# Kernel optimization log

Hardware: AMD Instinct MI355X
Metric: run time of the kernel (lower is better)

The kernel has to match this reference:

```python
import jax, jax.numpy as jnp
import numpy as np

NUM_HEADS = 12

def setup_inputs() -> dict:
    key = jax.random.key(0)
    k1, k2, k3, k4 = jax.random.split(key, 4)
    B, N, D = 8, 1024, 768
    x = jax.random.normal(k1, (B, N, D), dtype=jnp.float32)
    mask = jax.random.randint(k2, (B, N), 0, 2, dtype=jnp.int32)
    Wqkv = jax.random.normal(k3, (3 * D, D), dtype=jnp.float32) * (D ** -0.5)
    Wproj = jax.random.normal(k4, (D, D), dtype=jnp.float32) * (D ** -0.5)
    bproj = jnp.zeros((D,), dtype=jnp.float32)
    return {"x": x, "mask": mask, "Wqkv": Wqkv, "Wproj": Wproj, "bproj": bproj}

def reference(x, mask, Wqkv, Wproj, bproj):
    B, N, D = x.shape
    H = NUM_HEADS
    hd = D // H
    scale = hd ** -0.5
    # QKV projection (no bias), split into q,k,v of shape [B,H,N,hd]
    qkv = jnp.einsum('bnd,ed->bne', x, Wqkv).reshape(B, N, 3, H, hd)
    qkv = jnp.transpose(qkv, (2, 0, 3, 1, 4))
    q, k, v = qkv[0], qkv[1], qkv[2]
    # padding mask: attend where both query and key are valid; masked-out
    # (padded) query rows attend only to themselves (diagonal) to avoid NaNs
    m = mask.astype(bool)  # [B,N]
    pair = m[:, None, :, None] & m[:, None, None, :]          # [B,1,N,N]
    diag = jnp.eye(N, dtype=bool)[None, None]                 # [1,1,N,N]
    attn_mask = pair | (diag & ~m[:, None, :, None])          # [B,1,N,N]
    scores = jnp.einsum('bhnd,bhmd->bhnm', q, k) * scale      # [B,H,N,N]
    scores = jnp.where(attn_mask, scores, jnp.finfo(scores.dtype).min)
    attn = jax.nn.softmax(scores, axis=-1)
    out = jnp.einsum('bhnm,bhmd->bhnd', attn, v)
    out = jnp.transpose(out, (0, 2, 1, 3)).reshape(B, N, D)
    out = jnp.einsum('bnd,ed->bne', out, Wproj) + bproj
    return out
```

## Files before the change

### kernel.cpp

```cpp
#include <hip/hip_runtime.h>
#include <hip/hip_bf16.h>
#include <stdint.h>


typedef unsigned short u16;
typedef __attribute__((ext_vector_type(8))) short short8;
typedef __attribute__((ext_vector_type(4))) float f32x4;

#define MFMA16(a, b, c) __builtin_amdgcn_mfma_f32_16x16x32_bf16((a), (b), (c), 0, 0, 0)

static __device__ __forceinline__ float bf2f(u16 u) {
    return __uint_as_float(((unsigned int)u) << 16);
}
static __device__ __forceinline__ u16 f2bf(float f) {
    __hip_bfloat16 h = __float2bfloat16(f);
    return *(u16*)&h;
}
static __device__ __forceinline__ void gld16(const u16* g, u16* l) {
  __builtin_amdgcn_global_load_lds(
      (const __attribute__((address_space(1))) void*)g,
      (__attribute__((address_space(3))) void*)l, 16, 0, 0);
}

__global__ __launch_bounds__(256) void cvt_bf16(
    const float* __restrict__ s0, u16* __restrict__ d0, int n0,
    const float* __restrict__ s1, u16* __restrict__ d1, int n1,
    const float* __restrict__ s2, u16* __restrict__ d2, int n2) {
  int i = (blockIdx.x * 256 + threadIdx.x) * 4;
  const float* s; u16* d;
  if (i < n0) { s = s0 + i; d = d0 + i; }
  else if ((i -= n0) < n1) { s = s1 + i; d = d1 + i; }
  else if ((i -= n1) < n2) { s = s2 + i; d = d2 + i; }
  else return;
  float4 v = *(const float4*)s;
  ushort4 o;
  o.x = f2bf(v.x); o.y = f2bf(v.y); o.z = f2bf(v.z); o.w = f2bf(v.w);
  *(ushort4*)d = o;
}

template<int K, int LDC, bool BF16OUT>
__global__ __launch_bounds__(256) void gemm_bt(
    const u16* __restrict__ A,
    const u16* __restrict__ B,
    void* __restrict__ Cout,
    const float* __restrict__ bias) {
  __shared__ u16 As[128 * 32];
  __shared__ u16 Bs[128 * 32];
  const int tid = threadIdx.x;
  const int w = tid >> 6, l = tid & 63;
  const int lane16 = l & 15, quad = l >> 4;
  const int i0 = blockIdx.y * 128, j0 = blockIdx.x * 128;
  const int mh = (w & 1) * 64;
  const int nh = (w >> 1) * 64;

  f32x4 acc[4][4];
  #pragma unroll
  for (int mt = 0; mt < 4; mt++)
    #pragma unroll
    for (int nt = 0; nt < 4; nt++) acc[mt][nt] = (f32x4){0.f, 0.f, 0.f, 0.f};

  for (int kt = 0; kt < K / 32; kt++) {
    const int k0 = kt * 32;
    __syncthreads();
    #pragma unroll
    for (int s = 0; s < 2; s++) {
      int idx = tid + s * 256;
      int row = idx >> 2, c8 = (idx & 3) * 8;
      gld16(&A[(size_t)(i0 + row) * K + k0 + c8], &As[row * 32 + c8]);
      gld16(&B[(size_t)(j0 + row) * K + k0 + c8], &Bs[row * 32 + c8]);
    }
    __syncthreads();

    short8 af[4], bf[4];
    #pragma unroll
    for (int mt = 0; mt < 4; mt++)
      af[mt] = *(const short8*)&As[(mh + mt * 16 + lane16) * 32 + quad * 8];
    #pragma unroll
    for (int nt = 0; nt < 4; nt++)
      bf[nt] = *(const short8*)&Bs[(nh + nt * 16 + lane16) * 32 + quad * 8];
    #pragma unroll
    for (int mt = 0; mt < 4; mt++)
      #pragma unroll
      for (int nt = 0; nt < 4; nt++)
        acc[mt][nt] = MFMA16(af[mt], bf[nt], acc[mt][nt]);
  }

  #pragma unroll
  for (int mt = 0; mt < 4; mt++) {
    #pragma unroll
    for (int nt = 0; nt < 4; nt++) {
      int col = j0 + nh + nt * 16 + lane16;
      #pragma unroll
      for (int r = 0; r < 4; r++) {
        int row = i0 + mh + mt * 16 + quad * 4 + r;
        if (BF16OUT) {
          ((u16*)Cout)[(size_t)row * LDC + col] = f2bf(acc[mt][nt][r]);
        } else {
          ((float*)Cout)[(size_t)row * LDC + col] = acc[mt][nt][r] + bias[col];
        }
      }
    }
  }
}

__global__ __launch_bounds__(256, 4) void attn_mfma(
    const u16* __restrict__ qkv,
    const int* __restrict__ mask,
    u16* __restrict__ ctx) {
  __shared__ u16 Ks[64][72];
  __shared__ u16 Vt[64][72];
  __shared__ u16 Ps[4][32][72];
  __shared__ float mkb[64];
  __shared__ int mqs[128];

  const int tid = threadIdx.x;
  const int w = tid >> 6, l = tid & 63;
  const int lane16 = l & 15, quad = l >> 4;
  const int idx = blockIdx.x;
  const int bh = idx % 96;
  const int rb = idx / 96;
  const int b = bh / 12, h = bh % 12;
  const int n0 = rb * 128;
  const int baseRow = b * 1024;

  const int key_s = tid >> 2, ds_s = (tid & 3) * 16;
  const int kA_s = (tid & 31) * 2, dg_s = tid >> 5;

  if (tid < 128) mqs[tid] = mask[baseRow + n0 + tid];

  short8 qfrag[2][2];
  #pragma unroll
  for (int qt = 0; qt < 2; qt++) {
    const u16* qp = qkv + (size_t)(baseRow + n0 + w*32 + qt*16 + lane16) * 2304 + h*64;
    #pragma unroll
    for (int ks = 0; ks < 2; ks++)
      qfrag[qt][ks] = *(const short8*)(qp + ks*32 + quad*8);
  }

  f32x4 oacc[2][4];
  #pragma unroll
  for (int qt = 0; qt < 2; qt++)
    #pragma unroll
    for (int nt = 0; nt < 4; nt++) oacc[qt][nt] = (f32x4){0.f, 0.f, 0.f, 0.f};
  float lsum[2] = {0.f, 0.f};

  const float K1 = 0.18033688011112043f;
  const float K0 = -23.083120654223415f;

  for (int c = 0; c < 16; c++) {
    if (c) __syncthreads();
    {
      const u16* kp = qkv + (size_t)(baseRow + c*64 + key_s) * 2304 + 768 + h*64 + ds_s;
      uint4 kr0 = *(const uint4*)kp;
      uint4 kr1 = *(const uint4*)(kp + 8);
      const u16* vp = qkv + (size_t)(baseRow + c*64 + kA_s) * 2304 + 1536 + h*64 + dg_s*8;
      uint4 vr0 = *(const uint4*)vp;
      uint4 vr1 = *(const uint4*)(vp + 2304);
      *(uint4*)&Ks[key_s][ds_s]     = kr0;
      *(uint4*)&Ks[key_s][ds_s + 8] = kr1;
      const u16* va = (const u16*)&vr0;
      const u16* vb = (const u16*)&vr1;
      #pragma unroll
      for (int j = 0; j < 8; j++)
        *(unsigned int*)&Vt[dg_s*8 + j][kA_s] =
            (unsigned int)va[j] | ((unsigned int)vb[j] << 16);
      if (tid < 64) mkb[tid] = mask[baseRow + c*64 + tid] ? 0.f : -1e38f;
    }
    __syncthreads();

    f32x4 sacc[4][2];
    #pragma unroll
    for (int kt = 0; kt < 4; kt++)
      #pragma unroll
      for (int qt = 0; qt < 2; qt++) sacc[kt][qt] = (f32x4){0.f, 0.f, 0.f, 0.f};
    #pragma unroll
    for (int ks = 0; ks < 2; ks++) {
      short8 kf[4];
      #pragma unroll
      for (int kt = 0; kt < 4; kt++)
        kf[kt] = *(const short8*)&Ks[kt*16 + lane16][ks*32 + quad*8];
      #pragma unroll
      for (int kt = 0; kt < 4; kt++)
        #pragma unroll
        for (int qt = 0; qt < 2; qt++)
          sacc[kt][qt] = MFMA16(kf[kt], qfrag[qt][ks], sacc[kt][qt]);
    }

    #pragma unroll
    for (int kt = 0; kt < 4; kt++) {
      #pragma unroll
      for (int qt = 0; qt < 2; qt++) {
        u16 pk[4];
        #pragma unroll
        for (int r = 0; r < 4; r++) {
          int keyl = kt*16 + quad*4 + r;
          float e = __builtin_amdgcn_exp2f(fmaf(sacc[kt][qt][r], K1, K0) + mkb[keyl]);
          lsum[qt] += e;
          pk[r] = f2bf(e);
        }
        uint2 pv;
        pv.x = (unsigned int)pk[0] | ((unsigned int)pk[1] << 16);
        pv.y = (unsigned int)pk[2] | ((unsigned int)pk[3] << 16);
        *(uint2*)&Ps[w][qt*16 + lane16][kt*16 + quad*4] = pv;
      }
    }

    #pragma unroll
    for (int kc = 0; kc < 2; kc++) {
      short8 pf[2], vf[4];
      #pragma unroll
      for (int qt = 0; qt < 2; qt++)
        pf[qt] = *(const short8*)&Ps[w][qt*16 + lane16][kc*32 + quad*8];
      #pragma unroll
      for (int nt = 0; nt < 4; nt++)
        vf[nt] = *(const short8*)&Vt[nt*16 + lane16][kc*32 + quad*8];
      #pragma unroll
      for (int qt = 0; qt < 2; qt++)
        #pragma unroll
        for (int nt = 0; nt < 4; nt++)
          oacc[qt][nt] = MFMA16(pf[qt], vf[nt], oacc[qt][nt]);
    }
  }

  float linv[2][4];
  #pragma unroll
  for (int qt = 0; qt < 2; qt++) {
    float s = lsum[qt];
    s += __shfl_xor(s, 16);
    s += __shfl_xor(s, 32);
    #pragma unroll
    for (int r = 0; r < 4; r++)
      linv[qt][r] = 1.0f / __shfl(s, quad*4 + r);
  }
  #pragma unroll
  for (int qt = 0; qt < 2; qt++) {
    #pragma unroll
    for (int r = 0; r < 4; r++) {
      int rl = w*32 + qt*16 + quad*4 + r;
      int rg = n0 + rl;
      int mq = mqs[rl];
      #pragma unroll
      for (int nt = 0; nt < 4; nt++) {
        u16 outv;
        if (mq) {
          outv = f2bf(oacc[qt][nt][r] * linv[qt][r]);
        } else {
          outv = qkv[(size_t)(baseRow + rg) * 2304 + 1536 + h*64 + nt*16 + lane16];
        }
        ctx[(size_t)(baseRow + rg) * 768 + h*64 + nt*16 + lane16] = outv;
      }
    }
  }
}

extern "C" void kernel_launch(void* const* d_in, const int* in_sizes, int n_in,
                              void* d_out, int out_size, void* d_ws, size_t ws_size,
                              hipStream_t stream) {
  const float* x     = (const float*)d_in[0];
  const int*   mask  = (const int*)d_in[1];
  const float* Wqkv  = (const float*)d_in[2];
  const float* Wproj = (const float*)d_in[3];
  const float* bproj = (const float*)d_in[4];
  float* out = (float*)d_out;

  const int NX = 8192 * 768;
  const int NQ = 2304 * 768;
  const int NP = 768 * 768;

  char* wsb = (char*)d_ws;
  u16* qkv    = (u16*)wsb;
  u16* ctx    = (u16*)(wsb + (size_t)8192 * 2304 * 2);
  u16* xb     = (u16*)(wsb + (size_t)8192 * 2304 * 2 + (size_t)8192 * 768 * 2);
  u16* wqkvb  = xb + NX;
  u16* wprojb = wqkvb + NQ;

  int cvt_blocks = ((NX + NQ + NP) / 4 + 255) / 256;
  cvt_bf16<<<dim3(cvt_blocks), 256, 0, stream>>>(x, xb, NX, Wqkv, wqkvb, NQ, Wproj, wprojb, NP);

  gemm_bt<768, 2304, true><<<dim3(18, 64), 256, 0, stream>>>(xb, wqkvb, qkv, nullptr);
  attn_mfma<<<dim3(768), 256, 0, stream>>>(qkv, mask, ctx);
  gemm_bt<768, 768, false><<<dim3(6, 64), 256, 0, stream>>>(ctx, wprojb, out, bproj);
}
```

Measured before the change: 202.0 us.

## Fuse fp32-to-bf16 conversion into GEMM tile loads and drop separate convert kernel

Removes the standalone cvt_bf16 pass over x, Wqkv and Wproj. The GEMMs now load fp32 tiles directly into LDS and pack them to bf16 in registers before the MFMA. The projection GEMM is retiled to 128x64 with a bf16 A and fp32 B, which doubles its grid. This saves a kernel launch and the write and re-read of the bf16 copies. In exchange the QKV GEMM moves twice the bytes through LDS and runs extra conversion instructions in its inner loop, and Wqkv is converted repeatedly across blocks.

```diff
diff --git a/kernel.cpp b/kernel.cpp
--- a/kernel.cpp
+++ b/kernel.cpp
@@ -9,43 +9,32 @@
 
 #define MFMA16(a, b, c) __builtin_amdgcn_mfma_f32_16x16x32_bf16((a), (b), (c), 0, 0, 0)
 
-static __device__ __forceinline__ float bf2f(u16 u) {
-    return __uint_as_float(((unsigned int)u) << 16);
-}
 static __device__ __forceinline__ u16 f2bf(float f) {
     __hip_bfloat16 h = __float2bfloat16(f);
     return *(u16*)&h;
 }
-static __device__ __forceinline__ void gld16(const u16* g, u16* l) {
+static __device__ __forceinline__ void gld16(const void* g, void* l) {
   __builtin_amdgcn_global_load_lds(
       (const __attribute__((address_space(1))) void*)g,
       (__attribute__((address_space(3))) void*)l, 16, 0, 0);
 }
-
-__global__ __launch_bounds__(256) void cvt_bf16(
-    const float* __restrict__ s0, u16* __restrict__ d0, int n0,
-    const float* __restrict__ s1, u16* __restrict__ d1, int n1,
-    const float* __restrict__ s2, u16* __restrict__ d2, int n2) {
-  int i = (blockIdx.x * 256 + threadIdx.x) * 4;
-  const float* s; u16* d;
-  if (i < n0) { s = s0 + i; d = d0 + i; }
-  else if ((i -= n0) < n1) { s = s1 + i; d = d1 + i; }
-  else if ((i -= n1) < n2) { s = s2 + i; d = d2 + i; }
-  else return;
-  float4 v = *(const float4*)s;
-  ushort4 o;
-  o.x = f2bf(v.x); o.y = f2bf(v.y); o.z = f2bf(v.z); o.w = f2bf(v.w);
-  *(ushort4*)d = o;
-}
-
-template<int K, int LDC, bool BF16OUT>
-__global__ __launch_bounds__(256) void gemm_bt(
-    const u16* __restrict__ A,
-    const u16* __restrict__ B,
-    void* __restrict__ Cout,
-    const float* __restrict__ bias) {
-  __shared__ u16 As[128 * 32];
-  __shared__ u16 Bs[128 * 32];
+static __device__ __forceinline__ short8 pack_bf16x8(const float* p) {
+  float4 a = *(const float4*)p;
+  float4 b = *(const float4*)(p + 4);
+  short8 r;
+  r[0] = (short)f2bf(a.x); r[1] = (short)f2bf(a.y);
+  r[2] = (short)f2bf(a.z); r[3] = (short)f2bf(a.w);
+  r[4] = (short)f2bf(b.x); r[5] = (short)f2bf(b.y);
+  r[6] = (short)f2bf(b.z); r[7] = (short)f2bf(b.w);
+  return r;
+}
+
+__global__ __launch_bounds__(256) void gemm_qkv_f32(
+    const float* __restrict__ A,
+    const float* __restrict__ B,
+    u16* __restrict__ C) {
+  __shared__ float As[128 * 32];
+  __shared__ float Bs[128 * 32];
   const int tid = threadIdx.x;
   const int w = tid >> 6, l = tid & 63;
   const int lane16 = l & 15, quad = l >> 4;
@@ -59,45 +48,107 @@
     #pragma unroll
     for (int nt = 0; nt < 4; nt++) acc[mt][nt] = (f32x4){0.f, 0.f, 0.f, 0.f};
 
-  for (int kt = 0; kt < K / 32; kt++) {
+  for (int kt = 0; kt < 24; kt++) {
+    const int k0 = kt * 32;
+    __syncthreads();
+    #pragma unroll
+    for (int s = 0; s < 4; s++) {
+      int idx = tid + s * 256;
+      int row = idx >> 3, c4 = (idx & 7) * 4;
+      gld16(&A[(size_t)(i0 + row) * 768 + k0 + c4], &As[idx * 4]);
+      gld16(&B[(size_t)(j0 + row) * 768 + k0 + c4], &Bs[idx * 4]);
+    }
+    __syncthreads();
+
+    short8 af[4], bf[4];
+    #pragma unroll
+    for (int mt = 0; mt < 4; mt++)
+      af[mt] = pack_bf16x8(&As[(mh + mt * 16 + lane16) * 32 + quad * 8]);
+    #pragma unroll
+    for (int nt = 0; nt < 4; nt++)
+      bf[nt] = pack_bf16x8(&Bs[(nh + nt * 16 + lane16) * 32 + quad * 8]);
+    #pragma unroll
+    for (int mt = 0; mt < 4; mt++)
+      #pragma unroll
+      for (int nt = 0; nt < 4; nt++)
+        acc[mt][nt] = MFMA16(af[mt], bf[nt], acc[mt][nt]);
+  }
+
+  #pragma unroll
+  for (int mt = 0; mt < 4; mt++) {
+    #pragma unroll
+    for (int nt = 0; nt < 4; nt++) {
+      int col = j0 + nh + nt * 16 + lane16;
+      #pragma unroll
+      for (int r = 0; r < 4; r++) {
+        int row = i0 + mh + mt * 16 + quad * 4 + r;
+        C[(size_t)row * 2304 + col] = f2bf(acc[mt][nt][r]);
+      }
+    }
+  }
+}
+
+__global__ __launch_bounds__(256) void gemm_proj_mix(
+    const u16* __restrict__ A,
+    const float* __restrict__ B,
+    const float* __restrict__ bias,
+    float* __restrict__ Out) {
+  __shared__ u16 As[128 * 32];
+  __shared__ float Bs[64 * 32];
+  const int tid = threadIdx.x;
+  const int w = tid >> 6, l = tid & 63;
+  const int lane16 = l & 15, quad = l >> 4;
+  const int i0 = blockIdx.y * 128, j0 = blockIdx.x * 64;
+  const int mh = (w & 1) * 64;
+  const int nh = (w >> 1) * 32;
+
+  f32x4 acc[4][2];
+  #pragma unroll
+  for (int mt = 0; mt < 4; mt++)
+    #pragma unroll
+    for (int nt = 0; nt < 2; nt++) acc[mt][nt] = (f32x4){0.f, 0.f, 0.f, 0.f};
+
+  for (int kt = 0; kt < 24; kt++) {
     const int k0 = kt * 32;
     __syncthreads();
     #pragma unroll
     for (int s = 0; s < 2; s++) {
       int idx = tid + s * 256;
       int row = idx >> 2, c8 = (idx & 3) * 8;
-      gld16(&A[(size_t)(i0 + row) * K + k0 + c8], &As[row * 32 + c8]);
-      gld16(&B[(size_t)(j0 + row) * K + k0 + c8], &Bs[row * 32 + c8]);
-    }
-    __syncthreads();
-
-    short8 af[4], bf[4];
+      gld16(&A[(size_t)(i0 + row) * 768 + k0 + c8], &As[idx * 8]);
+    }
+    #pragma unroll
+    for (int s = 0; s < 2; s++) {
+      int idx = tid + s * 256;
+      int row = idx >> 3, c4 = (idx & 7) * 4;
+      gld16(&B[(size_t)(j0 + row) * 768 + k0 + c4], &Bs[idx * 4]);
+    }
+    __syncthreads();
+
+    short8 af[4], bf[2];
     #pragma unroll
     for (int mt = 0; mt < 4; mt++)
       af[mt] = *(const short8*)&As[(mh + mt * 16 + lane16) * 32 + quad * 8];
     #pragma unroll
-    for (int nt = 0; nt < 4; nt++)
-      bf[nt] = *(const short8*)&Bs[(nh + nt * 16 + lane16) * 32 + quad * 8];
+    for (int nt = 0; nt < 2; nt++)
+      bf[nt] = pack_bf16x8(&Bs[(nh + nt * 16 + lane16) * 32 + quad * 8]);
     #pragma unroll
     for (int mt = 0; mt < 4; mt++)
       #pragma unroll
-      for (int nt = 0; nt < 4; nt++)
+      for (int nt = 0; nt < 2; nt++)
         acc[mt][nt] = MFMA16(af[mt], bf[nt], acc[mt][nt]);
   }
 
   #pragma unroll
   for (int mt = 0; mt < 4; mt++) {
     #pragma unroll
-    for (int nt = 0; nt < 4; nt++) {
+    for (int nt = 0; nt < 2; nt++) {
       int col = j0 + nh + nt * 16 + lane16;
+      float bv = bias[col];
       #pragma unroll
       for (int r = 0; r < 4; r++) {
         int row = i0 + mh + mt * 16 + quad * 4 + r;
-        if (BF16OUT) {
-          ((u16*)Cout)[(size_t)row * LDC + col] = f2bf(acc[mt][nt][r]);
-        } else {
-          ((float*)Cout)[(size_t)row * LDC + col] = acc[mt][nt][r] + bias[col];
-        }
+        Out[(size_t)row * 768 + col] = acc[mt][nt][r] + bv;
       }
     }
   }
@@ -263,21 +314,11 @@
   const float* bproj = (const float*)d_in[4];
   float* out = (float*)d_out;
 
-  const int NX = 8192 * 768;
-  const int NQ = 2304 * 768;
-  const int NP = 768 * 768;
-
   char* wsb = (char*)d_ws;
-  u16* qkv    = (u16*)wsb;
-  u16* ctx    = (u16*)(wsb + (size_t)8192 * 2304 * 2);
-  u16* xb     = (u16*)(wsb + (size_t)8192 * 2304 * 2 + (size_t)8192 * 768 * 2);
-  u16* wqkvb  = xb + NX;
-  u16* wprojb = wqkvb + NQ;
-
-  int cvt_blocks = ((NX + NQ + NP) / 4 + 255) / 256;
-  cvt_bf16<<<dim3(cvt_blocks), 256, 0, stream>>>(x, xb, NX, Wqkv, wqkvb, NQ, Wproj, wprojb, NP);
-
-  gemm_bt<768, 2304, true><<<dim3(18, 64), 256, 0, stream>>>(xb, wqkvb, qkv, nullptr);
+  u16* qkv = (u16*)wsb;
+  u16* ctx = (u16*)(wsb + (size_t)8192 * 2304 * 2);
+
+  gemm_qkv_f32<<<dim3(18, 64), 256, 0, stream>>>(x, Wqkv, qkv);
   attn_mfma<<<dim3(768), 256, 0, stream>>>(qkv, mask, ctx);
-  gemm_bt<768, 768, false><<<dim3(6, 64), 256, 0, stream>>>(ctx, wprojb, out, bproj);
-}
+  gemm_proj_mix<<<dim3(12, 64), 256, 0, stream>>>(ctx, Wproj, bproj, out);
+}
```

After: 525.2 us. 2.6x slower.
